# Optimization experiments

Hardware: AMD Instinct MI355X
Metric: run time of the kernel (lower is better)

## Reference

```python
import jax, jax.numpy as jnp
import numpy as np
import math

B, N, D, H = 2, 96, 64, 4  # batch, num_nodes, d_model, num_heads
DK = D // H


def setup_inputs() -> dict:
    key = jax.random.key(0)
    ks = jax.random.split(key, 11)
    s = 0.02
    return {
        "state": jax.random.normal(ks[0], (B, N * N, D), jnp.float32),
        "w_lk": jax.random.normal(ks[1], (D, D), jnp.float32) * s,
        "b_lk": jax.random.normal(ks[2], (D,), jnp.float32) * s,
        "w_rk": jax.random.normal(ks[3], (D, D), jnp.float32) * s,
        "b_rk": jax.random.normal(ks[4], (D,), jnp.float32) * s,
        "w_lv": jax.random.normal(ks[5], (D, D), jnp.float32) * s,
        "b_lv": jax.random.normal(ks[6], (D,), jnp.float32) * s,
        "w_rv": jax.random.normal(ks[7], (D, D), jnp.float32) * s,
        "b_rv": jax.random.normal(ks[8], (D,), jnp.float32) * s,
        "w_out": jax.random.normal(ks[9], (D, D), jnp.float32) * s,
        "b_out": jax.random.normal(ks[10], (D,), jnp.float32) * s,
    }


def reference(state, w_lk, b_lk, w_rk, b_rk, w_lv, b_lv, w_rv, b_rv, w_out, b_out):
    b = state.shape[0]
    n = int(np.sqrt(state.shape[1]))
    d_model = state.shape[2]
    h, dk = H, d_model // H

    def lin(x, w, bias):  # torch nn.Linear: x @ W^T + b
        return x @ w.T + bias

    # project and view as [b, n, n, h, dk]
    lk = lin(state, w_lk, b_lk).reshape(b, n, n, h, dk)
    rk = lin(state, w_rk, b_rk).reshape(b, n, n, h, dk)
    lv = lin(state, w_lv, b_lv).reshape(b, n, n, h, dk)
    rv = lin(state, w_rv, b_rv).reshape(b, n, n, h, dk)

    # triangular edge-attention scores over intermediate node a
    scores = jnp.einsum('bxahd,bayhd->bxayh', lk, rk) / math.sqrt(dk)
    att = jax.nn.softmax(scores, axis=2)  # softmax over a

    # fused contraction: equivalent to val = lv[x,a]*rv[a,y] then sum_a att*val,
    # without materializing the O(n^3 * d) val tensor
    x = jnp.einsum('bxayh,bxahd,bayhd->bxyhd', att, lv, rv)

    x = x.reshape(b, n * n, d_model)
    return lin(x, w_out, b_out)
```

## Files before the change

kernel.cpp:

```cpp
#include <hip/hip_runtime.h>

#define TENS   1179648
#define HM     147456
#define T_ROWS 18432
#define NP_S   6

__global__ __launch_bounds__(256) void proj4_kernel(
    const float* __restrict__ state,
    const float* __restrict__ w0, const float* __restrict__ b0,
    const float* __restrict__ w1, const float* __restrict__ b1,
    const float* __restrict__ w2, const float* __restrict__ b2,
    const float* __restrict__ w3, const float* __restrict__ b3,
    float* __restrict__ o0, float* __restrict__ o1,
    float* __restrict__ o2, float* __restrict__ o3)
{
    __shared__ float sw[64 * 68];
    __shared__ float srow[32 * 64];
    __shared__ float sb[64];
    const int t = threadIdx.x;
    const int mat  = blockIdx.x & 3;
    const int row0 = (blockIdx.x >> 2) * 32;
    const float* w  = (mat == 0) ? w0 : (mat == 1) ? w1 : (mat == 2) ? w2 : w3;
    const float* bi = (mat == 0) ? b0 : (mat == 1) ? b1 : (mat == 2) ? b2 : b3;
    float* o        = (mat == 0) ? o0 : (mat == 1) ? o1 : (mat == 2) ? o2 : o3;

#pragma unroll
    for (int j = 0; j < 4; ++j) {
        const int s = t + j * 256;
        const int c = s >> 4, k4 = s & 15;
        *(float4*)&sw[c * 68 + k4 * 4] = *(const float4*)(w + s * 4);
    }
#pragma unroll
    for (int j = 0; j < 2; ++j) {
        const int s = t + j * 256;
        *(float4*)&srow[s * 4] = *(const float4*)(state + row0 * 64 + s * 4);
    }
    if (t < 64) sb[t] = bi[t];
    __syncthreads();

    const int c = t & 63, rg = t >> 6;
    float acc[8];
#pragma unroll
    for (int r = 0; r < 8; ++r) acc[r] = sb[c];
#pragma unroll
    for (int k4 = 0; k4 < 16; ++k4) {
        const float4 w4 = *(const float4*)&sw[c * 68 + k4 * 4];
#pragma unroll
        for (int r = 0; r < 8; ++r) {
            const float4 s4 = *(const float4*)&srow[(rg * 8 + r) * 64 + k4 * 4];
            acc[r] = fmaf(s4.x, w4.x, acc[r]);
            acc[r] = fmaf(s4.y, w4.y, acc[r]);
            acc[r] = fmaf(s4.z, w4.z, acc[r]);
            acc[r] = fmaf(s4.w, w4.w, acc[r]);
        }
    }
    const int b = row0 / 9216;
    const int rbat0 = row0 - b * 9216 + rg * 8;
    const int h = c >> 4, dk = c & 15;
    float* dp = o + (size_t)(b * 4 + h) * HM + (size_t)rbat0 * 16 + dk;
#pragma unroll
    for (int r = 0; r < 8; ++r)
        dp[r * 16] = acc[r];
}

__global__ __launch_bounds__(256) void fused_attn_kernel(
    const float* __restrict__ lk, const float* __restrict__ rk,
    const float* __restrict__ lv, const float* __restrict__ rv,
    float* __restrict__ nump, float* __restrict__ denp)
{
    __shared__ float lk_s[2176];
    __shared__ float lv_s[2176];
    __shared__ float rk_s[2560];
    __shared__ float rv_s[2560];

    const int t = threadIdx.x;
    const int j = blockIdx.x;
    const int bh = j & 7;
    const int r2 = j >> 3;
    const int sc = r2 % 6;
    const int tile = r2 / 6;
    const int xt = tile % 3, yt = tile / 3;
    const int x0 = xt * 32, y0 = yt * 32;
    const int a00 = sc * 16;
    const int xi2 = t & 15, yi2 = t >> 4;

    const float* plk = lk + (size_t)bh * HM;
    const float* prk = rk + (size_t)bh * HM;
    const float* plv = lv + (size_t)bh * HM;
    const float* prv = rv + (size_t)bh * HM;

    float4 a00v = {0.f,0.f,0.f,0.f}, a01v = a00v, a02v = a00v, a03v = a00v;
    float4 a10v = a00v, a11v = a00v, a12v = a00v, a13v = a00v;
    float4 a20v = a00v, a21v = a00v, a22v = a00v, a23v = a00v;
    float4 a30v = a00v, a31v = a00v, a32v = a00v, a33v = a00v;
    float d00 = 0.f, d01 = 0.f, d10 = 0.f, d11 = 0.f;

    for (int acx = 0; acx < 4; ++acx) {
        const int a0 = a00 + acx * 4;
        __syncthreads();
#pragma unroll
        for (int jj = 0; jj < 2; ++jj) {
            const int slot = t + jj * 256;
            const int xl = slot >> 4, rem = slot & 15;
            const int ai = rem >> 2, c4 = rem & 3;
            const int goff = ((x0 + xl) * 96 + a0 + ai) * 16 + c4 * 4;
            const int loff = ((xl & 1) * 16 + (xl >> 1)) * 68 + ai * 16 + c4 * 4;
            *(float4*)&lk_s[loff] = *(const float4*)(plk + goff);
            *(float4*)&lv_s[loff] = *(const float4*)(plv + goff);
        }
#pragma unroll
        for (int jj = 0; jj < 2; ++jj) {
            const int slot = t + jj * 256;
            const int ai = slot >> 7, rem = slot & 127;
            const int yl = rem >> 2, c4 = rem & 3;
            const int goff = ((a0 + ai) * 96 + y0 + yl) * 16 + c4 * 4;
            const int loff = ai * 640 + ((yl & 1) * 16 + (yl >> 1)) * 20 + c4 * 4;
            *(float4*)&rk_s[loff] = *(const float4*)(prk + goff);
            *(float4*)&rv_s[loff] = *(const float4*)(prv + goff);
        }
        __syncthreads();
#pragma unroll
        for (int ai = 0; ai < 4; ++ai) {
            const int lo0 = xi2 * 68 + ai * 16;
            const int lo1 = (16 + xi2) * 68 + ai * 16;
            const int ro0 = ai * 640 + yi2 * 20;
            const int ro1 = ai * 640 + (16 + yi2) * 20;
            const float4 ka0 = *(const float4*)&lk_s[lo0];
            const float4 ka1 = *(const float4*)&lk_s[lo0 + 4];
            const float4 ka2 = *(const float4*)&lk_s[lo0 + 8];
            const float4 ka3 = *(const float4*)&lk_s[lo0 + 12];
            const float4 kb0 = *(const float4*)&lk_s[lo1];
            const float4 kb1 = *(const float4*)&lk_s[lo1 + 4];
            const float4 kb2 = *(const float4*)&lk_s[lo1 + 8];
            const float4 kb3 = *(const float4*)&lk_s[lo1 + 12];
            const float4 qa0 = *(const float4*)&rk_s[ro0];
            const float4 qa1 = *(const float4*)&rk_s[ro0 + 4];
            const float4 qa2 = *(const float4*)&rk_s[ro0 + 8];
            const float4 qa3 = *(const float4*)&rk_s[ro0 + 12];
            const float4 qb0 = *(const float4*)&rk_s[ro1];
            const float4 qb1 = *(const float4*)&rk_s[ro1 + 4];
            const float4 qb2 = *(const float4*)&rk_s[ro1 + 8];
            const float4 qb3 = *(const float4*)&rk_s[ro1 + 12];

#define DOT16(A0,A1,A2,A3,B0,B1,B2,B3)                                   \
    fmaf(A3.w,B3.w, fmaf(A3.z,B3.z, fmaf(A3.y,B3.y, fmaf(A3.x,B3.x,     \
    fmaf(A2.w,B2.w, fmaf(A2.z,B2.z, fmaf(A2.y,B2.y, fmaf(A2.x,B2.x,     \
    fmaf(A1.w,B1.w, fmaf(A1.z,B1.z, fmaf(A1.y,B1.y, fmaf(A1.x,B1.x,     \
    fmaf(A0.w,B0.w, fmaf(A0.z,B0.z, fmaf(A0.y,B0.y, A0.x*B0.x)))))))))))))))
            const float s00 = DOT16(ka0,ka1,ka2,ka3, qa0,qa1,qa2,qa3);
            const float s01 = DOT16(ka0,ka1,ka2,ka3, qb0,qb1,qb2,qb3);
            const float s10 = DOT16(kb0,kb1,kb2,kb3, qa0,qa1,qa2,qa3);
            const float s11 = DOT16(kb0,kb1,kb2,kb3, qb0,qb1,qb2,qb3);
#undef DOT16
            const float p00 = __expf(s00 * 0.25f);
            const float p01 = __expf(s01 * 0.25f);
            const float p10 = __expf(s10 * 0.25f);
            const float p11 = __expf(s11 * 0.25f);
            d00 += p00; d01 += p01; d10 += p10; d11 += p11;

            const float4 la0 = *(const float4*)&lv_s[lo0];
            const float4 la1 = *(const float4*)&lv_s[lo0 + 4];
            const float4 la2 = *(const float4*)&lv_s[lo0 + 8];
            const float4 la3 = *(const float4*)&lv_s[lo0 + 12];
            const float4 lb0 = *(const float4*)&lv_s[lo1];
            const float4 lb1 = *(const float4*)&lv_s[lo1 + 4];
            const float4 lb2 = *(const float4*)&lv_s[lo1 + 8];
            const float4 lb3 = *(const float4*)&lv_s[lo1 + 12];
            const float4 va0 = *(const float4*)&rv_s[ro0];
            const float4 va1 = *(const float4*)&rv_s[ro0 + 4];
            const float4 va2 = *(const float4*)&rv_s[ro0 + 8];
            const float4 va3 = *(const float4*)&rv_s[ro0 + 12];
            const float4 vb0 = *(const float4*)&rv_s[ro1];
            const float4 vb1 = *(const float4*)&rv_s[ro1 + 4];
            const float4 vb2 = *(const float4*)&rv_s[ro1 + 8];
            const float4 vb3 = *(const float4*)&rv_s[ro1 + 12];

#define ACC4(AC, P, L, V)                       \
    AC.x = fmaf(P * L.x, V.x, AC.x);            \
    AC.y = fmaf(P * L.y, V.y, AC.y);            \
    AC.z = fmaf(P * L.z, V.z, AC.z);            \
    AC.w = fmaf(P * L.w, V.w, AC.w);
            ACC4(a00v, p00, la0, va0) ACC4(a01v, p00, la1, va1)
            ACC4(a02v, p00, la2, va2) ACC4(a03v, p00, la3, va3)
            ACC4(a10v, p01, la0, vb0) ACC4(a11v, p01, la1, vb1)
            ACC4(a12v, p01, la2, vb2) ACC4(a13v, p01, la3, vb3)
            ACC4(a20v, p10, lb0, va0) ACC4(a21v, p10, lb1, va1)
            ACC4(a22v, p10, lb2, va2) ACC4(a23v, p10, lb3, va3)
            ACC4(a30v, p11, lb0, vb0) ACC4(a31v, p11, lb1, vb1)
            ACC4(a32v, p11, lb2, vb2) ACC4(a33v, p11, lb3, vb3)
#undef ACC4
        }
    }

    const size_t pb = (size_t)(sc * 8 + bh) * 9216;
    const int xA = x0 + 2 * xi2, yA = y0 + 2 * yi2;
    {
        const size_t rb = pb + (size_t)xA * 96 + yA;
        float4* np = (float4*)(nump + rb * 16);
        np[0] = a00v; np[1] = a01v; np[2] = a02v; np[3] = a03v;
        denp[rb] = d00;
    }
    {
        const size_t rb = pb + (size_t)xA * 96 + yA + 1;
        float4* np = (float4*)(nump + rb * 16);
        np[0] = a10v; np[1] = a11v; np[2] = a12v; np[3] = a13v;
        denp[rb] = d01;
    }
    {
        const size_t rb = pb + (size_t)(xA + 1) * 96 + yA;
        float4* np = (float4*)(nump + rb * 16);
        np[0] = a20v; np[1] = a21v; np[2] = a22v; np[3] = a23v;
        denp[rb] = d10;
    }
    {
        const size_t rb = pb + (size_t)(xA + 1) * 96 + yA + 1;
        float4* np = (float4*)(nump + rb * 16);
        np[0] = a30v; np[1] = a31v; np[2] = a32v; np[3] = a33v;
        denp[rb] = d11;
    }
}

__global__ __launch_bounds__(256) void proj1_kernel(
    const float* __restrict__ nump, const float* __restrict__ denp,
    const float* __restrict__ w, const float* __restrict__ bi,
    float* __restrict__ out)
{
    __shared__ float sw[64 * 68];
    __shared__ float srow[32 * 64];
    __shared__ float sb[64];
    const int t = threadIdx.x;
    const int row0 = blockIdx.x * 32;

#pragma unroll
    for (int j = 0; j < 4; ++j) {
        const int s = t + j * 256;
        const int c = s >> 4, k4 = s & 15;
        *(float4*)&sw[c * 68 + k4 * 4] = *(const float4*)(w + s * 4);
    }
#pragma unroll
    for (int jj = 0; jj < 2; ++jj) {
        const int slot = t + jj * 256;
        const int rl = slot >> 4, hc = slot & 15;
        const int grow = row0 + rl;
        const int bb = grow / 9216;
        const int rb = grow - bb * 9216;
        const int bh = bb * 4 + (hc >> 2);
        const int c4 = hc & 3;
        float sx = 0.f, sy = 0.f, sz = 0.f, sww = 0.f, dd = 0.f;
#pragma unroll
        for (int sc = 0; sc < NP_S; ++sc) {
            const size_t rbs = (size_t)(sc * 8 + bh) * 9216 + rb;
            const float4 v = *(const float4*)(nump + rbs * 16 + c4 * 4);
            sx += v.x; sy += v.y; sz += v.z; sww += v.w;
            dd += denp[rbs];
        }
        const float inv = 1.0f / dd;
        float4 ov; ov.x = sx * inv; ov.y = sy * inv; ov.z = sz * inv; ov.w = sww * inv;
        *(float4*)&srow[rl * 64 + hc * 4] = ov;
    }
    if (t < 64) sb[t] = bi[t];
    __syncthreads();

    const int c = t & 63, rg = t >> 6;
    float acc[8];
#pragma unroll
    for (int r = 0; r < 8; ++r) acc[r] = sb[c];
#pragma unroll
    for (int k4 = 0; k4 < 16; ++k4) {
        const float4 w4 = *(const float4*)&sw[c * 68 + k4 * 4];
#pragma unroll
        for (int r = 0; r < 8; ++r) {
            const float4 s4 = *(const float4*)&srow[(rg * 8 + r) * 64 + k4 * 4];
            acc[r] = fmaf(s4.x, w4.x, acc[r]);
            acc[r] = fmaf(s4.y, w4.y, acc[r]);
            acc[r] = fmaf(s4.z, w4.z, acc[r]);
            acc[r] = fmaf(s4.w, w4.w, acc[r]);
        }
    }
#pragma unroll
    for (int r = 0; r < 8; ++r)
        out[(row0 + rg * 8 + r) * 64 + c] = acc[r];
}

extern "C" void kernel_launch(void* const* d_in, const int* in_sizes, int n_in,
                              void* d_out, int out_size, void* d_ws, size_t ws_size,
                              hipStream_t stream)
{
    const float* state = (const float*)d_in[0];
    const float* w_lk  = (const float*)d_in[1];
    const float* b_lk  = (const float*)d_in[2];
    const float* w_rk  = (const float*)d_in[3];
    const float* b_rk  = (const float*)d_in[4];
    const float* w_lv  = (const float*)d_in[5];
    const float* b_lv  = (const float*)d_in[6];
    const float* w_rv  = (const float*)d_in[7];
    const float* b_rv  = (const float*)d_in[8];
    const float* w_out = (const float*)d_in[9];
    const float* b_out = (const float*)d_in[10];
    float* out = (float*)d_out;

    float* ws = (float*)d_ws;
    float* lk   = ws;
    float* rk   = ws + (size_t)TENS;
    float* lv   = ws + (size_t)2 * TENS;
    float* rv   = ws + (size_t)3 * TENS;
    float* nump = ws + (size_t)4 * TENS;
    float* denp = nump + (size_t)NP_S * 8 * 9216 * 16;

    proj4_kernel<<<4 * (T_ROWS / 32), 256, 0, stream>>>(
        state, w_lk, b_lk, w_rk, b_rk, w_lv, b_lv, w_rv, b_rv, lk, rk, lv, rv);
    fused_attn_kernel<<<432, 256, 0, stream>>>(lk, rk, lv, rv, nump, denp);
    proj1_kernel<<<T_ROWS / 32, 256, 0, stream>>>(nump, denp, w_out, b_out, out);
}
```

Before: 139.4 us.

## Use register-blocked 4x8 outer-product tiles in projection kernels with 128-row blocks

Both linear-projection kernels now handle 128 rows per block instead of 32. The weight matrix is stored transposed in shared memory, and each thread computes a 4-column by 8-row register tile as an outer product. This raises arithmetic intensity per shared-memory load, amortises the weight staging across more rows, and lets results be written with float4 stores. The trade-off is more shared memory per block and a quarter as many blocks, which lowers occupancy and parallelism across the GPU.

```diff
diff --git a/kernel.cpp b/kernel.cpp
--- a/kernel.cpp
+++ b/kernel.cpp
@@ -14,12 +14,13 @@
     float* __restrict__ o0, float* __restrict__ o1,
     float* __restrict__ o2, float* __restrict__ o3)
 {
-    __shared__ float sw[64 * 68];
-    __shared__ float srow[32 * 64];
+    __shared__ float swt[64 * 68];
+    __shared__ float srow[128 * 68];
     __shared__ float sb[64];
     const int t = threadIdx.x;
-    const int mat  = blockIdx.x & 3;
-    const int row0 = (blockIdx.x >> 2) * 32;
+    const int mat = blockIdx.x & 3;
+    const int g   = blockIdx.x >> 2;
+    const int row0 = g * 128;
     const float* w  = (mat == 0) ? w0 : (mat == 1) ? w1 : (mat == 2) ? w2 : w3;
     const float* bi = (mat == 0) ? b0 : (mat == 1) ? b1 : (mat == 2) ? b2 : b3;
     float* o        = (mat == 0) ? o0 : (mat == 1) ? o1 : (mat == 2) ? o2 : o3;
@@ -28,39 +29,63 @@
     for (int j = 0; j < 4; ++j) {
         const int s = t + j * 256;
         const int c = s >> 4, k4 = s & 15;
-        *(float4*)&sw[c * 68 + k4 * 4] = *(const float4*)(w + s * 4);
-    }
-#pragma unroll
-    for (int j = 0; j < 2; ++j) {
+        const float4 wv = *(const float4*)(w + c * 64 + k4 * 4);
+        swt[(k4 * 4 + 0) * 68 + c] = wv.x;
+        swt[(k4 * 4 + 1) * 68 + c] = wv.y;
+        swt[(k4 * 4 + 2) * 68 + c] = wv.z;
+        swt[(k4 * 4 + 3) * 68 + c] = wv.w;
+    }
+#pragma unroll
+    for (int j = 0; j < 8; ++j) {
         const int s = t + j * 256;
-        *(float4*)&srow[s * 4] = *(const float4*)(state + row0 * 64 + s * 4);
+        const int row = s >> 4, k4 = s & 15;
+        *(float4*)&srow[row * 68 + k4 * 4] =
+            *(const float4*)(state + (size_t)(row0 + row) * 64 + k4 * 4);
     }
     if (t < 64) sb[t] = bi[t];
     __syncthreads();
 
-    const int c = t & 63, rg = t >> 6;
-    float acc[8];
-#pragma unroll
-    for (int r = 0; r < 8; ++r) acc[r] = sb[c];
+    const int c4 = t & 15, rg = t >> 4;
+    const float4 binit = *(const float4*)&sb[c4 * 4];
+    float4 acc[8];
+#pragma unroll
+    for (int rr = 0; rr < 8; ++rr) acc[rr] = binit;
+
 #pragma unroll
     for (int k4 = 0; k4 < 16; ++k4) {
-        const float4 w4 = *(const float4*)&sw[c * 68 + k4 * 4];
-#pragma unroll
-        for (int r = 0; r < 8; ++r) {
-            const float4 s4 = *(const float4*)&srow[(rg * 8 + r) * 64 + k4 * 4];
-            acc[r] = fmaf(s4.x, w4.x, acc[r]);
-            acc[r] = fmaf(s4.y, w4.y, acc[r]);
-            acc[r] = fmaf(s4.z, w4.z, acc[r]);
-            acc[r] = fmaf(s4.w, w4.w, acc[r]);
-        }
-    }
-    const int b = row0 / 9216;
-    const int rbat0 = row0 - b * 9216 + rg * 8;
-    const int h = c >> 4, dk = c & 15;
-    float* dp = o + (size_t)(b * 4 + h) * HM + (size_t)rbat0 * 16 + dk;
-#pragma unroll
-    for (int r = 0; r < 8; ++r)
-        dp[r * 16] = acc[r];
+        const float4 wq0 = *(const float4*)&swt[(k4 * 4 + 0) * 68 + c4 * 4];
+        const float4 wq1 = *(const float4*)&swt[(k4 * 4 + 1) * 68 + c4 * 4];
+        const float4 wq2 = *(const float4*)&swt[(k4 * 4 + 2) * 68 + c4 * 4];
+        const float4 wq3 = *(const float4*)&swt[(k4 * 4 + 3) * 68 + c4 * 4];
+#pragma unroll
+        for (int rr = 0; rr < 8; ++rr) {
+            const float4 s4 = *(const float4*)&srow[(rg + rr * 16) * 68 + k4 * 4];
+            acc[rr].x = fmaf(s4.x, wq0.x, acc[rr].x);
+            acc[rr].y = fmaf(s4.x, wq0.y, acc[rr].y);
+            acc[rr].z = fmaf(s4.x, wq0.z, acc[rr].z);
+            acc[rr].w = fmaf(s4.x, wq0.w, acc[rr].w);
+            acc[rr].x = fmaf(s4.y, wq1.x, acc[rr].x);
+            acc[rr].y = fmaf(s4.y, wq1.y, acc[rr].y);
+            acc[rr].z = fmaf(s4.y, wq1.z, acc[rr].z);
+            acc[rr].w = fmaf(s4.y, wq1.w, acc[rr].w);
+            acc[rr].x = fmaf(s4.z, wq2.x, acc[rr].x);
+            acc[rr].y = fmaf(s4.z, wq2.y, acc[rr].y);
+            acc[rr].z = fmaf(s4.z, wq2.z, acc[rr].z);
+            acc[rr].w = fmaf(s4.z, wq2.w, acc[rr].w);
+            acc[rr].x = fmaf(s4.w, wq3.x, acc[rr].x);
+            acc[rr].y = fmaf(s4.w, wq3.y, acc[rr].y);
+            acc[rr].z = fmaf(s4.w, wq3.z, acc[rr].z);
+            acc[rr].w = fmaf(s4.w, wq3.w, acc[rr].w);
+        }
+    }
+    const int b  = row0 / 9216;
+    const int h  = c4 >> 2;
+    const int dq = c4 & 3;
+    float* dp = o + (size_t)(b * 4 + h) * HM + dq * 4;
+    const int rb0 = row0 - b * 9216 + rg;
+#pragma unroll
+    for (int rr = 0; rr < 8; ++rr)
+        *(float4*)(dp + (size_t)(rb0 + rr * 16) * 16) = acc[rr];
 }
 
 __global__ __launch_bounds__(256) void fused_attn_kernel(
@@ -225,61 +250,82 @@
     const float* __restrict__ w, const float* __restrict__ bi,
     float* __restrict__ out)
 {
-    __shared__ float sw[64 * 68];
-    __shared__ float srow[32 * 64];
+    __shared__ float swt[64 * 68];
+    __shared__ float srow[128 * 68];
     __shared__ float sb[64];
     const int t = threadIdx.x;
-    const int row0 = blockIdx.x * 32;
+    const int row0 = blockIdx.x * 128;
+    const int bb  = row0 / 9216;
+    const int rb0 = row0 - bb * 9216;
 
 #pragma unroll
     for (int j = 0; j < 4; ++j) {
         const int s = t + j * 256;
         const int c = s >> 4, k4 = s & 15;
-        *(float4*)&sw[c * 68 + k4 * 4] = *(const float4*)(w + s * 4);
-    }
-#pragma unroll
-    for (int jj = 0; jj < 2; ++jj) {
-        const int slot = t + jj * 256;
-        const int rl = slot >> 4, hc = slot & 15;
-        const int grow = row0 + rl;
-        const int bb = grow / 9216;
-        const int rb = grow - bb * 9216;
+        const float4 wv = *(const float4*)(w + c * 64 + k4 * 4);
+        swt[(k4 * 4 + 0) * 68 + c] = wv.x;
+        swt[(k4 * 4 + 1) * 68 + c] = wv.y;
+        swt[(k4 * 4 + 2) * 68 + c] = wv.z;
+        swt[(k4 * 4 + 3) * 68 + c] = wv.w;
+    }
+#pragma unroll
+    for (int j = 0; j < 8; ++j) {
+        const int s = t + j * 256;
+        const int rl = s >> 4, hc = s & 15;
         const int bh = bb * 4 + (hc >> 2);
-        const int c4 = hc & 3;
-        float sx = 0.f, sy = 0.f, sz = 0.f, sww = 0.f, dd = 0.f;
+        const int c4g = hc & 3;
+        const int rb = rb0 + rl;
+        float sx = 0.f, sy = 0.f, sz = 0.f, sw4 = 0.f, dd = 0.f;
 #pragma unroll
         for (int sc = 0; sc < NP_S; ++sc) {
             const size_t rbs = (size_t)(sc * 8 + bh) * 9216 + rb;
-            const float4 v = *(const float4*)(nump + rbs * 16 + c4 * 4);
-            sx += v.x; sy += v.y; sz += v.z; sww += v.w;
+            const float4 v = *(const float4*)(nump + rbs * 16 + c4g * 4);
+            sx += v.x; sy += v.y; sz += v.z; sw4 += v.w;
             dd += denp[rbs];
         }
         const float inv = 1.0f / dd;
-        float4 ov; ov.x = sx * inv; ov.y = sy * inv; ov.z = sz * inv; ov.w = sww * inv;
-        *(float4*)&srow[rl * 64 + hc * 4] = ov;
+        float4 ov; ov.x = sx * inv; ov.y = sy * inv; ov.z = sz * inv; ov.w = sw4 * inv;
+        *(float4*)&srow[rl * 68 + hc * 4] = ov;
     }
     if (t < 64) sb[t] = bi[t];
     __syncthreads();
 
-    const int c = t & 63, rg = t >> 6;
-    float acc[8];
-#pragma unroll
-    for (int r = 0; r < 8; ++r) acc[r] = sb[c];
+    const int c4 = t & 15, rg = t >> 4;
+    const float4 binit = *(const float4*)&sb[c4 * 4];
+    float4 acc[8];
+#pragma unroll
+    for (int rr = 0; rr < 8; ++rr) acc[rr] = binit;
+
 #pragma unroll
     for (int k4 = 0; k4 < 16; ++k4) {
-        const float4 w4 = *(const float4*)&sw[c * 68 + k4 * 4];
-#pragma unroll
-        for (int r = 0; r < 8; ++r) {
-            const float4 s4 = *(const float4*)&srow[(rg * 8 + r) * 64 + k4 * 4];
-            acc[r] = fmaf(s4.x, w4.x, acc[r]);
-            acc[r] = fmaf(s4.y, w4.y, acc[r]);
-            acc[r] = fmaf(s4.z, w4.z, acc[r]);
-            acc[r] = fmaf(s4.w, w4.w, acc[r]);
-        }
-    }
-#pragma unroll
-    for (int r = 0; r < 8; ++r)
-        out[(row0 + rg * 8 + r) * 64 + c] = acc[r];
+        const float4 wq0 = *(const float4*)&swt[(k4 * 4 + 0) * 68 + c4 * 4];
+        const float4 wq1 = *(const float4*)&swt[(k4 * 4 + 1) * 68 + c4 * 4];
+        const float4 wq2 = *(const float4*)&swt[(k4 * 4 + 2) * 68 + c4 * 4];
+        const float4 wq3 = *(const float4*)&swt[(k4 * 4 + 3) * 68 + c4 * 4];
+#pragma unroll
+        for (int rr = 0; rr < 8; ++rr) {
+            const float4 s4 = *(const float4*)&srow[(rg + rr * 16) * 68 + k4 * 4];
+            acc[rr].x = fmaf(s4.x, wq0.x, acc[rr].x);
+            acc[rr].y = fmaf(s4.x, wq0.y, acc[rr].y);
+            acc[rr].z = fmaf(s4.x, wq0.z, acc[rr].z);
+            acc[rr].w = fmaf(s4.x, wq0.w, acc[rr].w);
+            acc[rr].x = fmaf(s4.y, wq1.x, acc[rr].x);
+            acc[rr].y = fmaf(s4.y, wq1.y, acc[rr].y);
+            acc[rr].z = fmaf(s4.y, wq1.z, acc[rr].z);
+            acc[rr].w = fmaf(s4.y, wq1.w, acc[rr].w);
+            acc[rr].x = fmaf(s4.z, wq2.x, acc[rr].x);
+            acc[rr].y = fmaf(s4.z, wq2.y, acc[rr].y);
+            acc[rr].z = fmaf(s4.z, wq2.z, acc[rr].z);
+            acc[rr].w = fmaf(s4.z, wq2.w, acc[rr].w);
+            acc[rr].x = fmaf(s4.w, wq3.x, acc[rr].x);
+            acc[rr].y = fmaf(s4.w, wq3.y, acc[rr].y);
+            acc[rr].z = fmaf(s4.w, wq3.z, acc[rr].z);
+            acc[rr].w = fmaf(s4.w, wq3.w, acc[rr].w);
+        }
+    }
+#pragma unroll
+    for (int rr = 0; rr < 8; ++rr)
+        *(float4*)(out + (size_t)(row0 + rg + rr * 16) * 64 + c4 * 4) = acc[rr];
 }
 
 extern "C" void kernel_launch(void* const* d_in, const int* in_sizes, int n_in,
@@ -307,8 +353,8 @@
     float* nump = ws + (size_t)4 * TENS;
     float* denp = nump + (size_t)NP_S * 8 * 9216 * 16;
 
-    proj4_kernel<<<4 * (T_ROWS / 32), 256, 0, stream>>>(
+    proj4_kernel<<<4 * (T_ROWS / 128), 256, 0, stream>>>(
         state, w_lk, b_lk, w_rk, b_rk, w_lv, b_lv, w_rv, b_rv, lk, rk, lv, rv);
     fused_attn_kernel<<<432, 256, 0, stream>>>(lk, rk, lv, rv, nump, denp);
-    proj1_kernel<<<T_ROWS / 32, 256, 0, stream>>>(nump, denp, w_out, b_out, out);
+    proj1_kernel<<<T_ROWS / 128, 256, 0, stream>>>(nump, denp, w_out, b_out, out);
 }
```

New measurement: 137.2 us. Within noise of the previous version (-1.5%).
